# Optimization experiments

Hardware: AMD Instinct MI355X
Metric: run time of the kernel (lower is better)

## Reference

```python
import jax, jax.numpy as jnp
import numpy as np

N_NODES = 100000
N_EDGES = 600000
D = 128
N_CLASSES = 16


def _degrees(idx, n):
    ones = jnp.ones(idx.shape[0], dtype=jnp.float32)
    return jax.ops.segment_sum(ones, idx, num_segments=n)


def graph_conv(src, dst, h, W, b):
    # DGL GraphConv, norm='both': D_out^{-1/2} A D_in^{-1/2} h W + b
    n = h.shape[0]
    deg_out = jnp.maximum(_degrees(src, n), 1.0)
    deg_in = jnp.maximum(_degrees(dst, n), 1.0)
    h = h * jax.lax.rsqrt(deg_out)[:, None]          # src-side norm
    h = h @ W                                         # dense transform
    msg = h[src]                                      # gather  [E, d]
    agg = jax.ops.segment_sum(msg, dst, num_segments=n)  # scatter-add
    agg = agg * jax.lax.rsqrt(deg_in)[:, None]        # dst-side norm
    return agg + b


def setup_inputs() -> dict:
    key = jax.random.key(0)
    ks = jax.random.split(key, 8)
    h = jax.random.normal(ks[0], (N_NODES, D), dtype=jnp.float32)
    src = jax.random.randint(ks[1], (N_EDGES,), 0, N_NODES)
    dst = jax.random.randint(ks[2], (N_EDGES,), 0, N_NODES)
    s = 1.0 / np.sqrt(D)
    W1 = jax.random.normal(ks[3], (D, D), dtype=jnp.float32) * s
    b1 = jnp.zeros((D,), dtype=jnp.float32)
    W2 = jax.random.normal(ks[4], (D, D), dtype=jnp.float32) * s
    b2 = jnp.zeros((D,), dtype=jnp.float32)
    Wc = jax.random.normal(ks[5], (D, N_CLASSES), dtype=jnp.float32) * s
    bc = jnp.zeros((N_CLASSES,), dtype=jnp.float32)
    return {"h": h, "src": src, "dst": dst, "W1": W1, "b1": b1,
            "W2": W2, "b2": b2, "Wc": Wc, "bc": bc}


def reference(h, src, dst, W1, b1, W2, b2, Wc, bc):
    h = jax.nn.relu(graph_conv(src, dst, h, W1, b1))
    h = jax.nn.relu(graph_conv(src, dst, h, W2, b2))
    return h @ Wc + bc
```

## Files before the change

### kernel.cpp

```cpp
#include <hip/hip_runtime.h>


typedef __attribute__((ext_vector_type(4))) _Float16 half4_t;
typedef __attribute__((ext_vector_type(16))) float floatx16;

__global__ __launch_bounds__(256) void count_kernel(
    const int* __restrict__ src, const int* __restrict__ dst,
    int* __restrict__ cntO, int* __restrict__ cntI,
    int* __restrict__ rank, int E)
{
    int t = blockIdx.x * blockDim.x + threadIdx.x;
    if (t < E) {
        atomicAdd(&cntO[src[t]], 1);
    } else if (t < 2 * E) {
        int e = t - E;
        rank[e] = atomicAdd(&cntI[dst[e]], 1);
    }
}

__global__ __launch_bounds__(256) void scan1_kernel(
    const int* __restrict__ cntI, const int* __restrict__ cntO,
    int* __restrict__ excl, int* __restrict__ bsum,
    float* __restrict__ rs_out, float* __restrict__ rs_in, int n)
{
    __shared__ int tmp[256];
    int i = blockIdx.x * 256 + threadIdx.x;
    int v = 0;
    if (i < n) {
        v = cntI[i];
        rs_in[i]  = rsqrtf(fmaxf((float)v, 1.0f));
        rs_out[i] = rsqrtf(fmaxf((float)cntO[i], 1.0f));
    }
    tmp[threadIdx.x] = v;
    __syncthreads();
    for (int off = 1; off < 256; off <<= 1) {
        int t = (threadIdx.x >= off) ? tmp[threadIdx.x - off] : 0;
        __syncthreads();
        tmp[threadIdx.x] += t;
        __syncthreads();
    }
    if (i < n) excl[i] = tmp[threadIdx.x] - v;
    if (threadIdx.x == 255) bsum[blockIdx.x] = tmp[255];
}

__global__ __launch_bounds__(1024) void scan2_kernel(int* __restrict__ bsum, int nb)
{
    __shared__ int tmp[1024];
    int t = threadIdx.x;
    int v = (t < nb) ? bsum[t] : 0;
    tmp[t] = v;
    __syncthreads();
    for (int off = 1; off < 1024; off <<= 1) {
        int x = (t >= off) ? tmp[t - off] : 0;
        __syncthreads();
        tmp[t] += x;
        __syncthreads();
    }
    if (t < nb) bsum[t] = tmp[t] - v;
}

__global__ __launch_bounds__(256) void scan3_kernel(
    int* __restrict__ excl, const int* __restrict__ bsum, int n)
{
    int i = blockIdx.x * 256 + threadIdx.x;
    if (i < n) excl[i] += bsum[blockIdx.x];
}

__global__ __launch_bounds__(256) void fill_kernel(
    const int* __restrict__ src, const int* __restrict__ dst,
    const int* __restrict__ rank, const int* __restrict__ starts,
    int* __restrict__ eidx, int E)
{
    int e = blockIdx.x * blockDim.x + threadIdx.x;
    if (e < E) {
        eidx[starts[dst[e]] + rank[e]] = src[e];
    }
}

__global__ __launch_bounds__(256) void wpack_kernel(
    const float* __restrict__ W1, const float* __restrict__ W2,
    _Float16* __restrict__ WB1, _Float16* __restrict__ WB2)
{
    int gid = blockIdx.x * 256 + threadIdx.x;
    int j = gid & 16383;
    int i   = j & 3;
    int col = (j >> 2) & 127;
    int g   = (j >> 9) & 1;
    int kt  = j >> 10;
    int k = kt * 8 + g * 4 + i;
    if (gid < 16384) WB1[j] = (_Float16)W1[k * 128 + col];
    else             WB2[j] = (_Float16)W2[k * 128 + col];
}

template <int MODE>
__global__ __launch_bounds__(256) void gemm_mfma(
    const void* __restrict__ Xv, const _Float16* __restrict__ WB,
    const float* __restrict__ rs_out, _Float16* __restrict__ T, int n)
{
    __shared__ _Float16 xa[128 * 128];
    char* xab = (char*)xa;

    const int tid  = threadIdx.x;
    const int lane = tid & 63;
    const int wv   = tid >> 6;
    const int m    = lane & 31;
    const int g    = lane >> 5;
    const int rbase = blockIdx.x * 128 + wv * 32;

    {
        const int C = (tid & 31) * 4;
        const int rsub = tid >> 5;
#pragma unroll
        for (int p = 0; p < 16; ++p) {
            int R = p * 8 + rsub;
            int row = blockIdx.x * 128 + R;
            half4_t a;
            if (row < n) {
                if (MODE == 0) {
                    const float* X = (const float*)Xv;
                    float s = rs_out[row];
                    float4 v = *(const float4*)&X[(size_t)row * 128 + C];
                    a[0] = (_Float16)(v.x * s);
                    a[1] = (_Float16)(v.y * s);
                    a[2] = (_Float16)(v.z * s);
                    a[3] = (_Float16)(v.w * s);
                } else {
                    const _Float16* X = (const _Float16*)Xv;
                    a = *(const half4_t*)&X[(size_t)row * 128 + C];
                }
            } else {
                a[0] = a[1] = a[2] = a[3] = (_Float16)0.f;
            }
            int byte = (R * 256 + C * 2) ^ ((R & 7) << 4);
            *(half4_t*)(xab + byte) = a;
        }
    }
    __syncthreads();

    floatx16 acc0 = {}, acc1 = {}, acc2 = {}, acc3 = {};
    const int arow = wv * 32 + m;
    const _Float16* wb = WB + (size_t)(g * 128 + m) * 4;

#pragma unroll 2
    for (int kt = 0; kt < 16; ++kt) {
        int cbyte = kt * 16 + g * 8;
        half4_t a = *(const half4_t*)(xab + ((arow * 256 + cbyte) ^ ((m & 7) << 4)));
        const _Float16* wk = wb + (size_t)kt * 1024;
        half4_t b0 = *(const half4_t*)(wk);
        half4_t b1 = *(const half4_t*)(wk + 128);
        half4_t b2 = *(const half4_t*)(wk + 256);
        half4_t b3 = *(const half4_t*)(wk + 384);
        acc0 = __builtin_amdgcn_mfma_f32_32x32x8f16(a, b0, acc0, 0, 0, 0);
        acc1 = __builtin_amdgcn_mfma_f32_32x32x8f16(a, b1, acc1, 0, 0, 0);
        acc2 = __builtin_amdgcn_mfma_f32_32x32x8f16(a, b2, acc2, 0, 0, 0);
        acc3 = __builtin_amdgcn_mfma_f32_32x32x8f16(a, b3, acc3, 0, 0, 0);
    }

#pragma unroll
    for (int rg = 0; rg < 16; ++rg) {
        int rd = (rg & 3) + 8 * (rg >> 2) + 4 * g;
        int orow = rbase + rd;
        if (orow < n) {
            _Float16* tp = T + (size_t)orow * 128 + m;
            tp[0]  = (_Float16)acc0[rg];
            tp[32] = (_Float16)acc1[rg];
            tp[64] = (_Float16)acc2[rg];
            tp[96] = (_Float16)acc3[rg];
        }
    }
}

template <int MODE>
__global__ __launch_bounds__(256) void gather_f16(
    const _Float16* __restrict__ T, const int* __restrict__ eidx,
    const int* __restrict__ starts, const float* __restrict__ rs_in,
    const float* __restrict__ rs_out, const float* __restrict__ bias,
    _Float16* __restrict__ Xout, int n, int E)
{
    int wave = (blockIdx.x * 256 + threadIdx.x) >> 6;
    int lane = threadIdx.x & 63;
    int q = lane >> 5;
    int t = lane & 31;
    int node = wave * 2 + q;
    if (node >= n) return;
    int s0 = starts[node];
    int s1 = (node + 1 < n) ? starts[node + 1] : E;

    float acc[4] = {0.f, 0.f, 0.f, 0.f};
    int j = s0;
    for (; j + 3 < s1; j += 4) {
        int4 s4 = *(const int4*)&eidx[j];
        half4_t va = *(const half4_t*)&T[(size_t)s4.x * 128 + t * 4];
        half4_t vb = *(const half4_t*)&T[(size_t)s4.y * 128 + t * 4];
        half4_t vc = *(const half4_t*)&T[(size_t)s4.z * 128 + t * 4];
        half4_t vd = *(const half4_t*)&T[(size_t)s4.w * 128 + t * 4];
#pragma unroll
        for (int i = 0; i < 4; ++i)
            acc[i] += ((float)va[i] + (float)vb[i]) + ((float)vc[i] + (float)vd[i]);
    }
    if (j + 1 < s1) {
        int sA = eidx[j], sB = eidx[j + 1];
        half4_t va = *(const half4_t*)&T[(size_t)sA * 128 + t * 4];
        half4_t vb = *(const half4_t*)&T[(size_t)sB * 128 + t * 4];
#pragma unroll
        for (int i = 0; i < 4; ++i) acc[i] += (float)va[i] + (float)vb[i];
        j += 2;
    }
    if (j < s1) {
        int sA = eidx[j];
        half4_t va = *(const half4_t*)&T[(size_t)sA * 128 + t * 4];
#pragma unroll
        for (int i = 0; i < 4; ++i) acc[i] += (float)va[i];
    }

    float ri = rs_in[node];
    float ro = (MODE == 0) ? rs_out[node] : 1.0f;
    float4 bv = *(const float4*)&bias[t * 4];
    float bb[4] = {bv.x, bv.y, bv.z, bv.w};
    half4_t o;
#pragma unroll
    for (int i = 0; i < 4; ++i) {
        float x = fmaxf(fmaf(acc[i], ri, bb[i]), 0.f) * ro;
        o[i] = (_Float16)x;
    }
    *(half4_t*)&Xout[(size_t)node * 128 + t * 4] = o;
}

__global__ __launch_bounds__(256) void classifier_kernel(
    const _Float16* __restrict__ X, const float* __restrict__ Wc,
    const float* __restrict__ bout, float* __restrict__ out, int n)
{
    __shared__ float wl[128 * 16];
    __shared__ _Float16 xs[16][128];
    const int tid = threadIdx.x;
    const int row0 = blockIdx.x * 16;
#pragma unroll
    for (int i0 = 0; i0 < 2; ++i0) {
        int i = tid + i0 * 256;
        ((float4*)wl)[i] = ((const float4*)Wc)[i];
    }
    {
        int r = tid >> 4, c8 = (tid & 15) * 8;
        int row = row0 + r;
        float4 v = make_float4(0.f, 0.f, 0.f, 0.f);
        if (row < n) v = *(const float4*)&X[(size_t)row * 128 + c8];
        *(float4*)&xs[r][c8] = v;
    }
    __syncthreads();
    int c = tid & 15, r = tid >> 4;
    float acc = 0.f;
#pragma unroll 4
    for (int k = 0; k < 128; k += 2) {
        float x0 = (float)xs[r][k];
        float x1 = (float)xs[r][k + 1];
        acc = fmaf(x0, wl[k * 16 + c], acc);
        acc = fmaf(x1, wl[(k + 1) * 16 + c], acc);
    }
    int row = row0 + r;
    if (row < n) out[(size_t)row * 16 + c] = acc + bout[c];
}

extern "C" void kernel_launch(void* const* d_in, const int* in_sizes, int n_in,
                              void* d_out, int out_size, void* d_ws, size_t ws_size,
                              hipStream_t stream)
{
    const float* h   = (const float*)d_in[0];
    const int*   src = (const int*)d_in[1];
    const int*   dst = (const int*)d_in[2];
    const float* W1  = (const float*)d_in[3];
    const float* b1  = (const float*)d_in[4];
    const float* W2  = (const float*)d_in[5];
    const float* b2  = (const float*)d_in[6];
    const float* Wc  = (const float*)d_in[7];
    const float* bc  = (const float*)d_in[8];
    float* out = (float*)d_out;

    const int n = in_sizes[0] / 128;
    const int E = in_sizes[1];
    const int nb = (n + 255) / 256;

    char* ws = (char*)d_ws;
    int*   cntO    = (int*)ws;
    int*   cntI    = cntO + n;
    int*   rank    = cntI + n;
    float* rs_out  = (float*)(rank + E);
    float* rs_in   = rs_out + n;
    int*   starts  = (int*)(rs_in + n);
    int*   bsum    = starts + n;
    int*   eidx    = bsum + 1024;
    _Float16* WB1  = (_Float16*)(eidx + E);
    _Float16* WB2  = WB1 + 16384;
    size_t off = ((size_t)((char*)(WB2 + 16384) - ws) + 255) & ~(size_t)255;
    _Float16* bufA = (_Float16*)(ws + off);
    _Float16* bufB = bufA + (size_t)n * 128;

    hipMemsetAsync(cntO, 0, (size_t)2 * n * sizeof(int), stream);
    count_kernel<<<(2 * E + 255) / 256, 256, 0, stream>>>(src, dst, cntO, cntI, rank, E);
    scan1_kernel<<<nb, 256, 0, stream>>>(cntI, cntO, starts, bsum, rs_out, rs_in, n);
    scan2_kernel<<<1, 1024, 0, stream>>>(bsum, nb);
    scan3_kernel<<<nb, 256, 0, stream>>>(starts, bsum, n);
    fill_kernel<<<(E + 255) / 256, 256, 0, stream>>>(src, dst, rank, starts, eidx, E);
    wpack_kernel<<<128, 256, 0, stream>>>(W1, W2, WB1, WB2);

    int gblocks = (n + 127) / 128;
    int ablocks = (n + 7) / 8;

    gemm_mfma<0><<<gblocks, 256, 0, stream>>>(h, WB1, rs_out, bufA, n);
    gather_f16<0><<<ablocks, 256, 0, stream>>>(bufA, eidx, starts, rs_in, rs_out, b1, bufB, n, E);

    gemm_mfma<1><<<gblocks, 256, 0, stream>>>(bufB, WB2, rs_out, bufA, n);
    gather_f16<1><<<ablocks, 256, 0, stream>>>(bufA, eidx, starts, rs_in, rs_out, b2, bufB, n, E);

    classifier_kernel<<<(n + 15) / 16, 256, 0, stream>>>(bufB, Wc, bc, out, n);
}
```

Baseline: 211.4 us.

## Fuse degree counting with first GEMM and move source norm into gather

The edge-degree counting kernel and the first MFMA GEMM become one launch, with a block-index split: the first CB blocks do atomic counting and the rest do GEMM tiles. This is possible because the source-side degree scaling is moved out of the GEMM and applied per edge in the first gather using rs_out of each source. The aim is to overlap the atomic-bound counting with the compute-bound GEMM and remove a serial dependency. In exchange, layer-1 gather does one extra scattered rs_out load per edge, and the gather tail loop is simplified to a single-edge loop.

```diff
diff --git a/kernel.cpp b/kernel.cpp
--- a/kernel.cpp
+++ b/kernel.cpp
@@ -3,20 +3,6 @@
 
 typedef __attribute__((ext_vector_type(4))) _Float16 half4_t;
 typedef __attribute__((ext_vector_type(16))) float floatx16;
-
-__global__ __launch_bounds__(256) void count_kernel(
-    const int* __restrict__ src, const int* __restrict__ dst,
-    int* __restrict__ cntO, int* __restrict__ cntI,
-    int* __restrict__ rank, int E)
-{
-    int t = blockIdx.x * blockDim.x + threadIdx.x;
-    if (t < E) {
-        atomicAdd(&cntO[src[t]], 1);
-    } else if (t < 2 * E) {
-        int e = t - E;
-        rank[e] = atomicAdd(&cntI[dst[e]], 1);
-    }
-}
 
 __global__ __launch_bounds__(256) void scan1_kernel(
     const int* __restrict__ cntI, const int* __restrict__ cntO,
@@ -93,9 +79,9 @@
 }
 
 template <int MODE>
-__global__ __launch_bounds__(256) void gemm_mfma(
-    const void* __restrict__ Xv, const _Float16* __restrict__ WB,
-    const float* __restrict__ rs_out, _Float16* __restrict__ T, int n)
+__device__ __forceinline__ void gemm_tile(
+    int bid, const void* __restrict__ Xv, const _Float16* __restrict__ WB,
+    _Float16* __restrict__ T, int n)
 {
     __shared__ _Float16 xa[128 * 128];
     char* xab = (char*)xa;
@@ -105,7 +91,7 @@
     const int wv   = tid >> 6;
     const int m    = lane & 31;
     const int g    = lane >> 5;
-    const int rbase = blockIdx.x * 128 + wv * 32;
+    const int rbase = bid * 128 + wv * 32;
 
     {
         const int C = (tid & 31) * 4;
@@ -113,17 +99,16 @@
 #pragma unroll
         for (int p = 0; p < 16; ++p) {
             int R = p * 8 + rsub;
-            int row = blockIdx.x * 128 + R;
+            int row = bid * 128 + R;
             half4_t a;
             if (row < n) {
                 if (MODE == 0) {
                     const float* X = (const float*)Xv;
-                    float s = rs_out[row];
                     float4 v = *(const float4*)&X[(size_t)row * 128 + C];
-                    a[0] = (_Float16)(v.x * s);
-                    a[1] = (_Float16)(v.y * s);
-                    a[2] = (_Float16)(v.z * s);
-                    a[3] = (_Float16)(v.w * s);
+                    a[0] = (_Float16)v.x;
+                    a[1] = (_Float16)v.y;
+                    a[2] = (_Float16)v.z;
+                    a[3] = (_Float16)v.w;
                 } else {
                     const _Float16* X = (const _Float16*)Xv;
                     a = *(const half4_t*)&X[(size_t)row * 128 + C];
@@ -170,7 +155,35 @@
     }
 }
 
-template <int MODE>
+__global__ __launch_bounds__(256) void fused1_kernel(
+    const float* __restrict__ h, const _Float16* __restrict__ WB1,
+    _Float16* __restrict__ T1,
+    const int* __restrict__ src, const int* __restrict__ dst,
+    int* __restrict__ cntO, int* __restrict__ cntI, int* __restrict__ rank,
+    int n, int E, int CB)
+{
+    int bid = blockIdx.x;
+    if (bid < CB) {
+        int t = bid * 256 + threadIdx.x;
+        if (t < E) {
+            atomicAdd(&cntO[src[t]], 1);
+        } else if (t < 2 * E) {
+            int e = t - E;
+            rank[e] = atomicAdd(&cntI[dst[e]], 1);
+        }
+    } else {
+        gemm_tile<0>(bid - CB, h, WB1, T1, n);
+    }
+}
+
+__global__ __launch_bounds__(256) void gemm2_kernel(
+    const _Float16* __restrict__ X, const _Float16* __restrict__ WB,
+    _Float16* __restrict__ T, int n)
+{
+    gemm_tile<1>(blockIdx.x, X, WB, T, n);
+}
+
+template <int PES, int NS>
 __global__ __launch_bounds__(256) void gather_f16(
     const _Float16* __restrict__ T, const int* __restrict__ eidx,
     const int* __restrict__ starts, const float* __restrict__ rs_in,
@@ -194,27 +207,32 @@
         half4_t vb = *(const half4_t*)&T[(size_t)s4.y * 128 + t * 4];
         half4_t vc = *(const half4_t*)&T[(size_t)s4.z * 128 + t * 4];
         half4_t vd = *(const half4_t*)&T[(size_t)s4.w * 128 + t * 4];
-#pragma unroll
-        for (int i = 0; i < 4; ++i)
-            acc[i] += ((float)va[i] + (float)vb[i]) + ((float)vc[i] + (float)vd[i]);
-    }
-    if (j + 1 < s1) {
-        int sA = eidx[j], sB = eidx[j + 1];
-        half4_t va = *(const half4_t*)&T[(size_t)sA * 128 + t * 4];
-        half4_t vb = *(const half4_t*)&T[(size_t)sB * 128 + t * 4];
-#pragma unroll
-        for (int i = 0; i < 4; ++i) acc[i] += (float)va[i] + (float)vb[i];
-        j += 2;
-    }
-    if (j < s1) {
+        if (PES) {
+            float ra = rs_out[s4.x], rb = rs_out[s4.y];
+            float rc = rs_out[s4.z], rd = rs_out[s4.w];
+#pragma unroll
+            for (int i = 0; i < 4; ++i) {
+                acc[i] = fmaf((float)va[i], ra, acc[i]);
+                acc[i] = fmaf((float)vb[i], rb, acc[i]);
+                acc[i] = fmaf((float)vc[i], rc, acc[i]);
+                acc[i] = fmaf((float)vd[i], rd, acc[i]);
+            }
+        } else {
+#pragma unroll
+            for (int i = 0; i < 4; ++i)
+                acc[i] += ((float)va[i] + (float)vb[i]) + ((float)vc[i] + (float)vd[i]);
+        }
+    }
+    for (; j < s1; ++j) {
         int sA = eidx[j];
         half4_t va = *(const half4_t*)&T[(size_t)sA * 128 + t * 4];
-#pragma unroll
-        for (int i = 0; i < 4; ++i) acc[i] += (float)va[i];
+        float ra = PES ? rs_out[sA] : 1.0f;
+#pragma unroll
+        for (int i = 0; i < 4; ++i) acc[i] = fmaf((float)va[i], ra, acc[i]);
     }
 
     float ri = rs_in[node];
-    float ro = (MODE == 0) ? rs_out[node] : 1.0f;
+    float ro = NS ? rs_out[node] : 1.0f;
     float4 bv = *(const float4*)&bias[t * 4];
     float bb[4] = {bv.x, bv.y, bv.z, bv.w};
     half4_t o;
@@ -294,22 +312,24 @@
     _Float16* bufA = (_Float16*)(ws + off);
     _Float16* bufB = bufA + (size_t)n * 128;
 
+    const int CB = (2 * E + 255) / 256;
+    const int GB = (n + 127) / 128;
+
     hipMemsetAsync(cntO, 0, (size_t)2 * n * sizeof(int), stream);
-    count_kernel<<<(2 * E + 255) / 256, 256, 0, stream>>>(src, dst, cntO, cntI, rank, E);
+    wpack_kernel<<<128, 256, 0, stream>>>(W1, W2, WB1, WB2);
+    fused1_kernel<<<CB + GB, 256, 0, stream>>>(h, WB1, bufA, src, dst,
+                                               cntO, cntI, rank, n, E, CB);
     scan1_kernel<<<nb, 256, 0, stream>>>(cntI, cntO, starts, bsum, rs_out, rs_in, n);
     scan2_kernel<<<1, 1024, 0, stream>>>(bsum, nb);
     scan3_kernel<<<nb, 256, 0, stream>>>(starts, bsum, n);
     fill_kernel<<<(E + 255) / 256, 256, 0, stream>>>(src, dst, rank, starts, eidx, E);
-    wpack_kernel<<<128, 256, 0, stream>>>(W1, W2, WB1, WB2);
-
-    int gblocks = (n + 127) / 128;
+
     int ablocks = (n + 7) / 8;
 
-    gemm_mfma<0><<<gblocks, 256, 0, stream>>>(h, WB1, rs_out, bufA, n);
-    gather_f16<0><<<ablocks, 256, 0, stream>>>(bufA, eidx, starts, rs_in, rs_out, b1, bufB, n, E);
-
-    gemm_mfma<1><<<gblocks, 256, 0, stream>>>(bufB, WB2, rs_out, bufA, n);
-    gather_f16<1><<<ablocks, 256, 0, stream>>>(bufA, eidx, starts, rs_in, rs_out, b2, bufB, n, E);
+    gather_f16<1, 1><<<ablocks, 256, 0, stream>>>(bufA, eidx, starts, rs_in, rs_out, b1, bufB, n, E);
+
+    gemm2_kernel<<<GB, 256, 0, stream>>>(bufB, WB2, bufA, n);
+    gather_f16<0, 0><<<ablocks, 256, 0, stream>>>(bufA, eidx, starts, rs_in, rs_out, b2, bufB, n, E);
 
     classifier_kernel<<<(n + 15) / 16, 256, 0, stream>>>(bufB, Wc, bc, out, n);
 }
```

Result: no change. 210.6 us (-0.4%).
